# Kernel optimization log

Hardware: AMD Instinct MI355X
Metric: run time of the kernel (lower is better)

The kernel has to match this reference:

```python
import jax, jax.numpy as jnp
import numpy as np

VOCAB = 50257
D_MODEL = 1024
BATCH = 4
SEQ = 4096


def setup_inputs() -> dict:
    key = jax.random.key(0)
    k_ids, k_w = jax.random.split(key)
    input = jax.random.randint(k_ids, (BATCH, SEQ), 0, VOCAB, dtype=jnp.int32)
    # Linear(vocab, d_model, bias=False) weight: [d_model, vocab]
    W = jax.random.normal(k_w, (D_MODEL, VOCAB), dtype=jnp.float32) * (1.0 / np.sqrt(VOCAB))
    return {"input": input, "W": W}


def reference(input, W):
    # one_hot(input, vocab) @ W.T  ==  gather columns of W
    # out[b, s, :] = W[:, input[b, s]]  -> shape [B, S, d_model]
    return jnp.take(W.T, input, axis=0)
```

## Files before the change

kernel.cpp:

```cpp
#include <hip/hip_runtime.h>
#include <stdint.h>

#define VOCAB   50257
#define DMODEL  1024
#define VWIN    256
#define NB      ((VOCAB + VWIN - 1) / VWIN)
#define DCHUNK  32

#define WS_COUNT   0
#define WS_START   256
#define WS_CURSOR  768
#define WS_PERM    1024

__global__ __launch_bounds__(256) void hist_kernel(
    const int* __restrict__ ids, int* __restrict__ ws, int n_tokens)
{
    int t = blockIdx.x * 256 + threadIdx.x;
    if (t < n_tokens) {
        int id = ids[t];
        atomicAdd(&ws[WS_COUNT + (id >> 8)], 1);
    }
}

__global__ __launch_bounds__(256) void scan_kernel(int* __restrict__ ws)
{
    __shared__ int s[256];
    int tid = threadIdx.x;
    int c = (tid < NB) ? ws[WS_COUNT + tid] : 0;
    s[tid] = c;
    __syncthreads();
    for (int off = 1; off < 256; off <<= 1) {
        int v = (tid >= off) ? s[tid - off] : 0;
        __syncthreads();
        s[tid] += v;
        __syncthreads();
    }
    if (tid == 0) ws[WS_START + 0] = 0;
    ws[WS_START + tid + 1] = s[tid];
}

__global__ __launch_bounds__(256) void scatter_kernel(
    const int* __restrict__ ids, int* __restrict__ ws, int n_tokens)
{
    int t = blockIdx.x * 256 + threadIdx.x;
    if (t < n_tokens) {
        int id = ids[t];
        int b  = id >> 8;
        int pos = ws[WS_START + b] + atomicAdd(&ws[WS_CURSOR + b], 1);
        ws[WS_PERM + pos] = (int)(((uint32_t)id << 16) | (uint32_t)t);
    }
}

__global__ __launch_bounds__(256) void emit_kernel(
    const float* __restrict__ W, const int* __restrict__ ws,
    float* __restrict__ out)
{
    __shared__ float tile[DCHUNK][VWIN + 1];

    const int vwin = blockIdx.x;
    const int d0   = blockIdx.y * DCHUNK;
    const int v0   = vwin << 8;
    const int tid  = threadIdx.x;

    const float* Wbase = W + (size_t)d0 * VOCAB + v0;
    const int limit = VOCAB - v0;
    if (limit >= VWIN) {
        for (int e = tid * 4; e < DCHUNK * VWIN; e += 256 * 4) {
            int r = e >> 8, c = e & 255;
            float4 v = *(const float4*)(Wbase + (size_t)r * VOCAB + c);
            tile[r][c]     = v.x;
            tile[r][c + 1] = v.y;
            tile[r][c + 2] = v.z;
            tile[r][c + 3] = v.w;
        }
    } else {
        for (int e = tid * 4; e < DCHUNK * VWIN; e += 256 * 4) {
            int r = e >> 8, c = e & 255;
#pragma unroll
            for (int j = 0; j < 4; j++)
                tile[r][c + j] = (c + j < limit)
                    ? Wbase[(size_t)r * VOCAB + c + j] : 0.0f;
        }
    }
    __syncthreads();

    const int begin = ws[WS_START + vwin];
    const int end   = ws[WS_START + vwin + 1];
    const int lane  = tid & 63;
    const int w     = tid >> 6;
    const int g     = lane >> 3;
    const int dsub  = (lane & 7) << 2;

    for (int i = begin + w * 8; i < end; i += 32) {
        int idx = i + g;
        if (idx < end) {
            uint32_t packed = (uint32_t)ws[WS_PERM + idx];
            int t   = (int)(packed & 0xFFFFu);
            int col = (int)(packed >> 16) - v0;
            float4 v;
            v.x = tile[dsub][col];
            v.y = tile[dsub + 1][col];
            v.z = tile[dsub + 2][col];
            v.w = tile[dsub + 3][col];
            *(float4*)(out + (size_t)t * DMODEL + d0 + dsub) = v;
        }
    }
}

extern "C" void kernel_launch(void* const* d_in, const int* in_sizes, int n_in,
                              void* d_out, int out_size, void* d_ws, size_t ws_size,
                              hipStream_t stream) {
    const int*   ids = (const int*)d_in[0];
    const float* W   = (const float*)d_in[1];
    float*       out = (float*)d_out;
    int*         ws  = (int*)d_ws;

    const int n_tokens = in_sizes[0];
    const int nblk = (n_tokens + 255) / 256;

    hipMemsetAsync(ws, 0, 1024 * sizeof(int), stream);
    hist_kernel<<<nblk, 256, 0, stream>>>(ids, ws, n_tokens);
    scan_kernel<<<1, 256, 0, stream>>>(ws);
    scatter_kernel<<<nblk, 256, 0, stream>>>(ids, ws, n_tokens);

    dim3 grid(NB, DMODEL / DCHUNK);
    emit_kernel<<<grid, 256, 0, stream>>>(W, ws, out);
}
```

Before: 334.5 us.

## Use per-block shared-memory histograms and cursors instead of global atomics

The bucket sort over token ids now runs on 16 blocks. Each block builds its histogram in shared memory and writes per-block counts laid out bucket-major. The scan computes an exclusive prefix over all bucket-by-block counts, so scatter can use shared-memory cursors instead of global atomics. This also removes the memset. The aim is to cut global atomic contention and per-launch overhead in the preprocessing kernels, at the cost of running hist and scatter on only 16 blocks.

Measured after the change: 320.1 us. 1.04x faster.

```diff
diff --git a/kernel.cpp b/kernel.cpp
--- a/kernel.cpp
+++ b/kernel.cpp
@@ -6,28 +6,45 @@
 #define VWIN    256
 #define NB      ((VOCAB + VWIN - 1) / VWIN)
 #define DCHUNK  32
+#define HBLK    16
+#define NTOT    (NB * HBLK)
 
-#define WS_COUNT   0
-#define WS_START   256
-#define WS_CURSOR  768
-#define WS_PERM    1024
+#define WS_COUNT  0
+#define WS_START  4096
+#define WS_PERM   8192
 
 __global__ __launch_bounds__(256) void hist_kernel(
     const int* __restrict__ ids, int* __restrict__ ws, int n_tokens)
 {
-    int t = blockIdx.x * 256 + threadIdx.x;
-    if (t < n_tokens) {
-        int id = ids[t];
-        atomicAdd(&ws[WS_COUNT + (id >> 8)], 1);
-    }
+    __shared__ int h[NB];
+    const int tid = threadIdx.x, blk = blockIdx.x;
+    for (int i = tid; i < NB; i += 256) h[i] = 0;
+    __syncthreads();
+    const int per = (n_tokens + HBLK - 1) / HBLK;
+    const int t0 = blk * per;
+    const int t1 = min(n_tokens, t0 + per);
+    for (int t = t0 + tid; t < t1; t += 256)
+        atomicAdd(&h[ids[t] >> 8], 1);
+    __syncthreads();
+    for (int i = tid; i < NB; i += 256)
+        ws[WS_COUNT + i * HBLK + blk] = h[i];
 }
 
 __global__ __launch_bounds__(256) void scan_kernel(int* __restrict__ ws)
 {
     __shared__ int s[256];
-    int tid = threadIdx.x;
-    int c = (tid < NB) ? ws[WS_COUNT + tid] : 0;
-    s[tid] = c;
+    const int tid = threadIdx.x;
+    const int CH = (NTOT + 255) / 256;
+    const int base = tid * CH;
+    int vals[(NTOT + 255) / 256];
+    int sum = 0;
+#pragma unroll
+    for (int j = 0; j < CH; j++) {
+        int idx = base + j;
+        int v = (idx < NTOT) ? ws[WS_COUNT + idx] : 0;
+        vals[j] = v; sum += v;
+    }
+    s[tid] = sum;
     __syncthreads();
     for (int off = 1; off < 256; off <<= 1) {
         int v = (tid >= off) ? s[tid - off] : 0;
@@ -35,18 +52,31 @@
         s[tid] += v;
         __syncthreads();
     }
-    if (tid == 0) ws[WS_START + 0] = 0;
-    ws[WS_START + tid + 1] = s[tid];
+    int run = (tid > 0) ? s[tid - 1] : 0;
+#pragma unroll
+    for (int j = 0; j < CH; j++) {
+        int idx = base + j;
+        if (idx < NTOT) ws[WS_START + idx] = run;
+        run += vals[j];
+    }
+    if (tid == 255) ws[WS_START + NTOT] = run;
 }
 
 __global__ __launch_bounds__(256) void scatter_kernel(
     const int* __restrict__ ids, int* __restrict__ ws, int n_tokens)
 {
-    int t = blockIdx.x * 256 + threadIdx.x;
-    if (t < n_tokens) {
+    __shared__ int cur[NB];
+    const int tid = threadIdx.x, blk = blockIdx.x;
+    for (int i = tid; i < NB; i += 256)
+        cur[i] = ws[WS_START + i * HBLK + blk];
+    __syncthreads();
+    const int per = (n_tokens + HBLK - 1) / HBLK;
+    const int t0 = blk * per;
+    const int t1 = min(n_tokens, t0 + per);
+    for (int t = t0 + tid; t < t1; t += 256) {
         int id = ids[t];
         int b  = id >> 8;
-        int pos = ws[WS_START + b] + atomicAdd(&ws[WS_CURSOR + b], 1);
+        int pos = atomicAdd(&cur[b], 1);
         ws[WS_PERM + pos] = (int)(((uint32_t)id << 16) | (uint32_t)t);
     }
 }
@@ -84,8 +114,8 @@
     }
     __syncthreads();
 
-    const int begin = ws[WS_START + vwin];
-    const int end   = ws[WS_START + vwin + 1];
+    const int begin = ws[WS_START + vwin * HBLK];
+    const int end   = ws[WS_START + (vwin + 1) * HBLK];
     const int lane  = tid & 63;
     const int w     = tid >> 6;
     const int g     = lane >> 3;
@@ -116,12 +146,10 @@
     int*         ws  = (int*)d_ws;
 
     const int n_tokens = in_sizes[0];
-    const int nblk = (n_tokens + 255) / 256;
 
-    hipMemsetAsync(ws, 0, 1024 * sizeof(int), stream);
-    hist_kernel<<<nblk, 256, 0, stream>>>(ids, ws, n_tokens);
+    hist_kernel<<<HBLK, 256, 0, stream>>>(ids, ws, n_tokens);
     scan_kernel<<<1, 256, 0, stream>>>(ws);
-    scatter_kernel<<<nblk, 256, 0, stream>>>(ids, ws, n_tokens);
+    scatter_kernel<<<HBLK, 256, 0, stream>>>(ids, ws, n_tokens);
 
     dim3 grid(NB, DMODEL / DCHUNK);
     emit_kernel<<<grid, 256, 0, stream>>>(W, ws, out);
```
